# Kernel optimization log

Measured on AMD Instinct MI355X. Metric: run time of the kernel, lower is better.

Reference implementation:

```python
import jax, jax.numpy as jnp
import numpy as np

K = 2          # kernel_size
NQ = K * K     # 4 qubits, one per patch pixel
DIM = 2 ** NQ  # 16-dim statevector

def _cnot_ring_np():
    # fixed entangler: CNOT(0,1) CNOT(1,2) CNOT(2,3) CNOT(3,0), qubit 0 = MSB
    U = np.eye(DIM)
    def cnot(ctrl, tgt):
        M = np.zeros((DIM, DIM))
        for b in range(DIM):
            bits = [(b >> (NQ - 1 - q)) & 1 for q in range(NQ)]
            if bits[ctrl]:
                bits[tgt] ^= 1
            b2 = sum(bit << (NQ - 1 - q) for q, bit in enumerate(bits))
            M[b2, b] = 1.0
        return M
    for c, t in [(0, 1), (1, 2), (2, 3), (3, 0)]:
        U = cnot(c, t) @ U
    return U.astype(np.float32)

CNOT_RING = jnp.asarray(_cnot_ring_np())

def _sign_table_np():
    # ZSIGN[q, b] = +1 if bit q of basis state b is 0 else -1  (for <Z_q>)
    S = np.empty((NQ, DIM), np.float32)
    for q in range(NQ):
        for b in range(DIM):
            S[q, b] = 1.0 if ((b >> (NQ - 1 - q)) & 1) == 0 else -1.0
    return S

ZSIGN = jnp.asarray(_sign_table_np())

def _ry(theta):
    c, s = jnp.cos(theta / 2), jnp.sin(theta / 2)
    return jnp.stack([jnp.stack([c, -s], -1), jnp.stack([s, c], -1)], -2)

def _param_unitary(w):  # w: (NQ,) -> (DIM, DIM) real unitary
    u = _ry(w[0])
    for q in range(1, NQ):
        u = jnp.kron(u, _ry(w[q]))
    return CNOT_RING @ u

def setup_inputs() -> dict:
    key = jax.random.key(0)
    k1, k2 = jax.random.split(key)
    inputs = jax.random.uniform(k1, (64, 1, 224, 224), dtype=jnp.float32)
    weight = jax.random.uniform(k2, (1, NQ), dtype=jnp.float32) * (2 * jnp.pi)
    return {"inputs": inputs, "weight": weight}

def reference(inputs, weight):
    B, C, H, W = inputs.shape
    Lx, Ly = H - K + 1, W - K + 1
    # sliding KxK patches, angle-encoded: theta (B,C,Lx,Ly,NQ)
    theta = jnp.pi * jnp.stack(
        [inputs[:, :, dx:dx + Lx, dy:dy + Ly] for dx in range(K) for dy in range(K)],
        axis=-1)
    c, s = jnp.cos(theta / 2), jnp.sin(theta / 2)
    # product state RY(theta_q)|0000>: (B,C,Lx,Ly,DIM), all-real amplitudes
    psi = jnp.einsum('...a,...b,...c,...d->...abcd',
                     jnp.stack([c[..., 0], s[..., 0]], -1),
                     jnp.stack([c[..., 1], s[..., 1]], -1),
                     jnp.stack([c[..., 2], s[..., 2]], -1),
                     jnp.stack([c[..., 3], s[..., 3]], -1)
                     ).reshape(B, C, Lx, Ly, DIM)
    U = jax.vmap(_param_unitary)(weight)              # (C, DIM, DIM)
    psi = jnp.einsum('cij,bcxyj->bcxyi', U, psi)
    probs = psi * psi                                  # Born rule (real state)
    expz = jnp.einsum('bcxyk,qk->bcqxy', probs, ZSIGN)  # (B,C,NQ,Lx,Ly)
    return expz.reshape(B, C * NQ, Lx, Ly)
```

## Files before the change

kernel.cpp:

```cpp
#include <hip/hip_runtime.h>


constexpr int H = 224, W = 224;
constexpr int LX = 223, LY = 223;
constexpr long long PLANE = (long long)LX * LY;

__global__ __launch_bounds__(256) void quanv_kernel(
    const float* __restrict__ in,
    const float* __restrict__ wt,
    float* __restrict__ out)
{
    __shared__ float cw[4], sw[4];
    if (threadIdx.x < 4) {
        float s, c;
        sincosf(wt[threadIdx.x], &s, &c);
        sw[threadIdx.x] = s;
        cw[threadIdx.x] = c;
    }
    __syncthreads();

    const int y = threadIdx.x;
    const int x = blockIdx.x;
    const int b = blockIdx.y;
    if (y >= LY) return;

    const float* p = in + ((size_t)b * H + x) * W + y;
    const float v00 = p[0];
    const float v01 = p[1];
    const float v10 = p[W];
    const float v11 = p[W + 1];

    float s0, c0, s1, c1, s2, c2, s3, c3;
    sincospif(v00, &s0, &c0);
    sincospif(v01, &s1, &c1);
    sincospif(v10, &s2, &c2);
    sincospif(v11, &s3, &c3);

    const float z0 = fmaf(c0, cw[0], -(s0 * sw[0]));
    const float z1 = fmaf(c1, cw[1], -(s1 * sw[1]));
    const float z2 = fmaf(c2, cw[2], -(s2 * sw[2]));
    const float z3 = fmaf(c3, cw[3], -(s3 * sw[3]));

    const float o1 = z0 * z1;
    const float o2 = o1 * z2;
    const float o3 = o2 * z3;
    const float o0 = z1 * (z2 * z3);

    float* o = out + (size_t)b * 4 * PLANE + (size_t)x * LY + y;
    o[0]         = o0;
    o[PLANE]     = o1;
    o[2 * PLANE] = o2;
    o[3 * PLANE] = o3;
}

extern "C" void kernel_launch(void* const* d_in, const int* in_sizes, int n_in,
                              void* d_out, int out_size, void* d_ws, size_t ws_size,
                              hipStream_t stream) {
    const float* in = (const float*)d_in[0];
    const float* wt = (const float*)d_in[1];
    float* out = (float*)d_out;

    const int B = in_sizes[0] / (H * W);
    dim3 grid(LX, B);
    quanv_kernel<<<grid, 256, 0, stream>>>(in, wt, out);
}
```

Measured before the change: 86.38 us.

## Flatten grid to 1D and replace sincospi with fused cos-of-sum polynomial

Each qubit expectation factor c*cw - s*sw is rewritten as a single cosine of the summed angle, evaluated by a custom range-reduced minimax sine polynomial via the double-angle identity. This drops four sincospif calls and the shared-memory weight setup and barrier. The launch becomes a flat 1D grid over all output pixels, so no lanes sit idle the way they did when 223-wide rows ran in 256-thread blocks. In exchange each thread pays integer div/mod index math, and the polynomial may lose some accuracy compared with the library functions.

```diff
diff --git a/kernel.cpp b/kernel.cpp
--- a/kernel.cpp
+++ b/kernel.cpp
@@ -3,43 +3,51 @@
 
 constexpr int H = 224, W = 224;
 constexpr int LX = 223, LY = 223;
-constexpr long long PLANE = (long long)LX * LY;
+constexpr int PLANE = LX * LY;
+
+__device__ __forceinline__ float cos2pi(float u) {
+    float uf = u - rintf(u);
+    float t  = uf * 3.14159265358979f;
+    float t2 = t * t;
+    float q = -2.5052108e-8f;
+    q = fmaf(q, t2,  2.7557319e-6f);
+    q = fmaf(q, t2, -1.9841270e-4f);
+    q = fmaf(q, t2,  8.3333333e-3f);
+    q = fmaf(q, t2, -0.16666667f);
+    float s = fmaf(t * t2, q, t);
+    return fmaf(-2.0f * s, s, 1.0f);
+}
 
 __global__ __launch_bounds__(256) void quanv_kernel(
     const float* __restrict__ in,
     const float* __restrict__ wt,
-    float* __restrict__ out)
+    float* __restrict__ out,
+    int total)
 {
-    __shared__ float cw[4], sw[4];
-    if (threadIdx.x < 4) {
-        float s, c;
-        sincosf(wt[threadIdx.x], &s, &c);
-        sw[threadIdx.x] = s;
-        cw[threadIdx.x] = c;
-    }
-    __syncthreads();
+    const int n = blockIdx.x * 256 + threadIdx.x;
+    if (n >= total) return;
 
-    const int y = threadIdx.x;
-    const int x = blockIdx.x;
-    const int b = blockIdx.y;
-    if (y >= LY) return;
+    const int b = n / PLANE;
+    const int r = n - b * PLANE;
+    const int x = r / LY;
+    const int y = r - x * LY;
 
     const float* p = in + ((size_t)b * H + x) * W + y;
-    const float v00 = p[0];
-    const float v01 = p[1];
-    const float v10 = p[W];
-    const float v11 = p[W + 1];
+    const float v0 = p[0];
+    const float v1 = p[1];
+    const float v2 = p[W];
+    const float v3 = p[W + 1];
 
-    float s0, c0, s1, c1, s2, c2, s3, c3;
-    sincospif(v00, &s0, &c0);
-    sincospif(v01, &s1, &c1);
-    sincospif(v10, &s2, &c2);
-    sincospif(v11, &s3, &c3);
+    constexpr float inv2pi = 0.15915494309189535f;
+    const float w0 = wt[0] * inv2pi;
+    const float w1 = wt[1] * inv2pi;
+    const float w2 = wt[2] * inv2pi;
+    const float w3 = wt[3] * inv2pi;
 
-    const float z0 = fmaf(c0, cw[0], -(s0 * sw[0]));
-    const float z1 = fmaf(c1, cw[1], -(s1 * sw[1]));
-    const float z2 = fmaf(c2, cw[2], -(s2 * sw[2]));
-    const float z3 = fmaf(c3, cw[3], -(s3 * sw[3]));
+    const float z0 = cos2pi(fmaf(v0, 0.5f, w0));
+    const float z1 = cos2pi(fmaf(v1, 0.5f, w1));
+    const float z2 = cos2pi(fmaf(v2, 0.5f, w2));
+    const float z3 = cos2pi(fmaf(v3, 0.5f, w3));
 
     const float o1 = z0 * z1;
     const float o2 = o1 * z2;
@@ -47,10 +55,10 @@
     const float o0 = z1 * (z2 * z3);
 
     float* o = out + (size_t)b * 4 * PLANE + (size_t)x * LY + y;
-    o[0]         = o0;
-    o[PLANE]     = o1;
-    o[2 * PLANE] = o2;
-    o[3 * PLANE] = o3;
+    o[0]             = o0;
+    o[PLANE]         = o1;
+    o[2 * PLANE]     = o2;
+    o[3 * PLANE]     = o3;
 }
 
 extern "C" void kernel_launch(void* const* d_in, const int* in_sizes, int n_in,
@@ -61,6 +69,7 @@
     float* out = (float*)d_out;
 
     const int B = in_sizes[0] / (H * W);
-    dim3 grid(LX, B);
-    quanv_kernel<<<grid, 256, 0, stream>>>(in, wt, out);
+    const int total = B * PLANE;
+    const int grid = (total + 255) / 256;
+    quanv_kernel<<<grid, 256, 0, stream>>>(in, wt, out, total);
 }
```

New measurement: 81.32 us. -5.9%, faster.
